# Performance work log

Measured on AMD Instinct MI355X. Metric: run time of the kernel, lower is better.

The kernel has to match this reference:

```python
import jax, jax.numpy as jnp
import numpy as np

B, S, D = 2, 4096, 1024

def setup_inputs() -> dict:
    key = jax.random.key(0)
    k1, k2 = jax.random.split(key)
    x = jax.random.normal(k1, (B, S, D), dtype=jnp.float32)
    W = jax.random.normal(k2, (D, 3 * D), dtype=jnp.float32) * (1.0 / np.sqrt(D))
    b = jnp.zeros((3 * D,), dtype=jnp.float32)
    return {"x": x, "W": W, "b": b}

def reference(x, W, b) -> jnp.ndarray:
    D_ = x.shape[-1]
    qkv = x @ W + b                       # [B, S, 3D]
    q, k, v = jnp.split(qkv, 3, axis=2)    # each [B, S, D]
    scale = 1.0 / jnp.sqrt(jnp.asarray(D_, dtype=x.dtype))
    scores = jnp.einsum('bqd,bkd->bqk', q, k) * scale  # [B, S, S]
    weights = jax.nn.softmax(scores, axis=-1)
    return jnp.einsum('bqk,bkd->bqd', weights, v)       # [B, S, D]
```

## Files before the change

kernel.cpp:

```cpp
#include <hip/hip_runtime.h>
#include <hip/hip_bf16.h>

typedef __attribute__((ext_vector_type(4))) float  f32x4;
typedef __attribute__((ext_vector_type(8))) __bf16 bf16x8;
typedef __attribute__((ext_vector_type(8))) unsigned short u16x8;

typedef const __attribute__((address_space(1))) void gas_void;
typedef __attribute__((address_space(3))) void las_void;

__device__ __forceinline__ unsigned short f2bf(float x) {
    unsigned u = __builtin_bit_cast(unsigned, x);
    u += 0x7fffu + ((u >> 16) & 1u);
    return (unsigned short)(u >> 16);
}
__device__ __forceinline__ float bf2f(unsigned short h) {
    unsigned u = ((unsigned)h) << 16;
    return __builtin_bit_cast(float, u);
}
__device__ __forceinline__ void gload_lds16(const void* g, void* l) {
    __builtin_amdgcn_global_load_lds((gas_void*)g, (las_void*)l, 16, 0, 0);
}

#define WAITVM(N) asm volatile("s_waitcnt vmcnt(" #N ")" ::: "memory")

__global__ void k_f32_to_bf16(const float* __restrict__ in,
                              unsigned short* __restrict__ out, int n4) {
    int i = blockIdx.x * blockDim.x + threadIdx.x;
    if (i < n4) {
        float4 v = ((const float4*)in)[i];
        ushort4 o;
        o.x = f2bf(v.x); o.y = f2bf(v.y); o.z = f2bf(v.z); o.w = f2bf(v.w);
        ((ushort4*)out)[i] = o;
    }
}

__global__ void k_transpose_w(const float* __restrict__ W,
                              unsigned short* __restrict__ Wt,
                              int K, int N) {
    __shared__ unsigned short tile[32][33];
    int n0 = blockIdx.x * 32, k0 = blockIdx.y * 32;
    int tx = threadIdx.x, ty = threadIdx.y;
#pragma unroll
    for (int i = 0; i < 4; i++) {
        int kk = ty + i * 8;
        tile[kk][tx] = f2bf(W[(size_t)(k0 + kk) * N + n0 + tx]);
    }
    __syncthreads();
#pragma unroll
    for (int i = 0; i < 4; i++) {
        int nn = ty + i * 8;
        Wt[(size_t)(n0 + nn) * K + k0 + tx] = tile[tx][nn];
    }
}

__global__ void k_transpose_v(const unsigned short* __restrict__ Vrow,
                              unsigned short* __restrict__ Vt) {
    __shared__ unsigned short tile[32][33];
    int b = blockIdx.z;
    int s0 = blockIdx.x * 32, d0 = blockIdx.y * 32;
    int tx = threadIdx.x, ty = threadIdx.y;
#pragma unroll
    for (int i = 0; i < 4; i++) {
        int ss = ty + i * 8;
        tile[ss][tx] = Vrow[((size_t)(b * 4096 + s0 + ss)) * 1024 + d0 + tx];
    }
    __syncthreads();
#pragma unroll
    for (int i = 0; i < 4; i++) {
        int dd = ty + i * 8;
        Vt[((size_t)b * 1024 + d0 + dd) * 4096 + s0 + tx] = tile[tx][dd];
    }
}

template <int MODE>
__global__ __launch_bounds__(512, 2) void k_g256(
        const unsigned short* __restrict__ A, int lda,
        const unsigned short* __restrict__ Bt, int ldb,
        void* __restrict__ C, int ldc,
        unsigned short* __restrict__ Vp,
        const float* __restrict__ bias,
        int K, float alpha, long sA, long sB, long sC) {
    __shared__ __align__(16) unsigned short As[2][16384];
    __shared__ __align__(16) unsigned short Bs[2][16384];

    const int z = blockIdx.z;
    A  += (size_t)z * sA;
    Bt += (size_t)z * sB;

    const int nwg  = gridDim.x * gridDim.y;
    const int flat = blockIdx.y * gridDim.x + blockIdx.x;
    const int swzb = (flat & 7) * (nwg >> 3) + (flat >> 3);
    const int m0   = (swzb / gridDim.x) * 256;
    const int n0   = (swzb % gridDim.x) * 256;

    const int tid  = threadIdx.x;
    const int lane = tid & 63;
    const int wid  = tid >> 6;
    const int wm   = wid >> 2;
    const int wn   = wid & 3;
    const int l15  = lane & 15;
    const int l4   = lane >> 4;

    f32x4 acc[8][4] = {};

    const int srow = wid * 8 + (lane >> 3);
    const int kel  = (((lane & 7) ^ (lane >> 3)) << 3);
    const int c0 = ((l4 << 4)) ^ ((l15 & 7) << 4);
    const int c1 = (64 + (l4 << 4)) ^ ((l15 & 7) << 4);

    auto stageA = [&](int b, int h, int kt) {
#pragma unroll
        for (int c = 0; c < 2; c++) {
            const int r = h * 128 + c * 64 + srow;
            gload_lds16(A + (size_t)(m0 + r) * lda + kt * 64 + kel,
                        (char*)As + b * 32768 + h * 16384 + c * 8192 + (wid << 10));
        }
    };
    auto stageB = [&](int b, int h, int kt) {
#pragma unroll
        for (int c = 0; c < 2; c++) {
            const int r = h * 128 + c * 64 + srow;
            gload_lds16(Bt + (size_t)(n0 + r) * ldb + kt * 64 + kel,
                        (char*)Bs + b * 32768 + h * 16384 + c * 8192 + (wid << 10));
        }
    };

#define MM(I, J, X, Y) \
    acc[I][J] = __builtin_amdgcn_mfma_f32_16x16x32_bf16((X), (Y), acc[I][J], 0, 0, 0)

    const int NT = K >> 6;
    stageA(0, 0, 0); stageB(0, 0, 0); stageA(0, 1, 0); stageB(0, 1, 0);

    for (int t = 0; t < NT; t++) {
        const int cur = t & 1, nxt = cur ^ 1;
        const char* Ab = (const char*)As + cur * 32768;
        const char* Bb = (const char*)Bs + cur * 32768;

        if (t + 1 < NT) {
            stageA(nxt, 0, t + 1); stageB(nxt, 0, t + 1);
            WAITVM(4);
        } else {
            WAITVM(0);
        }
        __builtin_amdgcn_s_barrier();
        __builtin_amdgcn_sched_barrier(0);

        bf16x8 bfrg[2][2][2];
#pragma unroll
        for (int qn = 0; qn < 2; qn++)
#pragma unroll
        for (int nf = 0; nf < 2; nf++) {
            const int rb = (wn * 64 + qn * 32 + nf * 16 + l15) * 128;
            bfrg[qn][nf][0] = *(const bf16x8*)(Bb + rb + c0);
            bfrg[qn][nf][1] = *(const bf16x8*)(Bb + rb + c1);
        }
        {
            bf16x8 af[4][2];
#pragma unroll
            for (int mf = 0; mf < 4; mf++) {
                const int ra = (wm * 128 + 0 * 64 + mf * 16 + l15) * 128;
                af[mf][0] = *(const bf16x8*)(Ab + ra + c0);
                af[mf][1] = *(const bf16x8*)(Ab + ra + c1);
            }
            __builtin_amdgcn_s_setprio(1);
#pragma unroll
            for (int mf = 0; mf < 4; mf++)
#pragma unroll
            for (int qn = 0; qn < 2; qn++)
#pragma unroll
            for (int nf = 0; nf < 2; nf++) {
                MM(mf, qn * 2 + nf, af[mf][0], bfrg[qn][nf][0]);
                MM(mf, qn * 2 + nf, af[mf][1], bfrg[qn][nf][1]);
            }
            __builtin_amdgcn_s_setprio(0);
        }

        if (t + 1 < NT) { stageA(nxt, 1, t + 1); stageB(nxt, 1, t + 1); }
        {
            bf16x8 af[4][2];
#pragma unroll
            for (int mf = 0; mf < 4; mf++) {
                const int ra = (wm * 128 + 1 * 64 + mf * 16 + l15) * 128;
                af[mf][0] = *(const bf16x8*)(Ab + ra + c0);
                af[mf][1] = *(const bf16x8*)(Ab + ra + c1);
            }
            __builtin_amdgcn_s_setprio(1);
#pragma unroll
            for (int mf = 0; mf < 4; mf++)
#pragma unroll
            for (int qn = 0; qn < 2; qn++)
#pragma unroll
            for (int nf = 0; nf < 2; nf++) {
                MM(4 + mf, qn * 2 + nf, af[mf][0], bfrg[qn][nf][0]);
                MM(4 + mf, qn * 2 + nf, af[mf][1], bfrg[qn][nf][1]);
            }
            __builtin_amdgcn_s_setprio(0);
        }
        __builtin_amdgcn_s_barrier();
        __builtin_amdgcn_sched_barrier(0);
    }
#undef MM

#pragma unroll
    for (int qm = 0; qm < 2; qm++)
#pragma unroll
    for (int mf = 0; mf < 4; mf++) {
        const int row = m0 + wm * 128 + qm * 64 + mf * 16 + l4 * 4;
#pragma unroll
        for (int qn = 0; qn < 2; qn++)
#pragma unroll
        for (int nf = 0; nf < 2; nf++) {
            const int col = n0 + wn * 64 + qn * 32 + nf * 16 + l15;
            const float bv = (MODE == 2) ? bias[col] : 0.0f;
            const f32x4 av = acc[qm * 4 + mf][qn * 2 + nf];
#pragma unroll
            for (int r = 0; r < 4; r++) {
                const float v = av[r] * alpha + bv;
                if (MODE == 1) {
                    ((unsigned short*)C)[(size_t)z * sC + (size_t)(row + r) * ldc + col] = f2bf(v);
                } else {
                    const int lc = col & 1023;
                    if (col < 2048)
                        ((unsigned short*)C)[(size_t)(col >> 10) * 8388608 +
                                             (size_t)(row + r) * 1024 + lc] = f2bf(v);
                    else
                        Vp[(size_t)(row + r) * 1024 + lc] = f2bf(v);
                }
            }
        }
    }
}

__global__ void k_gemm_bt_f32(const unsigned short* __restrict__ A, int lda,
                              const unsigned short* __restrict__ Bt, int ldb,
                              float* __restrict__ C, int ldc,
                              int K, long sA, long sB, long sC) {
    __shared__ __align__(16) unsigned short As[128 * 32];
    __shared__ __align__(16) unsigned short Bs[128 * 32];

    const int z = blockIdx.z;
    A  += (size_t)z * sA;
    Bt += (size_t)z * sB;

    const int nwg  = gridDim.x * gridDim.y;
    const int flat = blockIdx.y * gridDim.x + blockIdx.x;
    const int swzb = (flat & 7) * (nwg >> 3) + (flat >> 3);
    const int m0   = (swzb / gridDim.x) * 128;
    const int n0   = (swzb % gridDim.x) * 128;

    const int tid  = threadIdx.x;
    const int lane = tid & 63;
    const int w    = tid >> 6;
    const int wr   = w >> 1, wc = w & 1;

    f32x4 acc[4][4] = {};
    const int r0  = lane >> 2;
    const int cEl = (lane & 3) * 8;

    for (int k0 = 0; k0 < K; k0 += 32) {
#pragma unroll
        for (int i = 0; i < 2; i++) {
            const int c = w + 4 * i;
            gload_lds16(A + (size_t)(m0 + c * 16 + r0) * lda + k0 + cEl,
                        (void*)(As + c * 512));
        }
#pragma unroll
        for (int i = 0; i < 2; i++) {
            const int c = w + 4 * i;
            gload_lds16(Bt + (size_t)(n0 + c * 16 + r0) * ldb + k0 + cEl,
                        (void*)(Bs + c * 512));
        }
        __syncthreads();

        bf16x8 af[4], bfr[4];
#pragma unroll
        for (int m = 0; m < 4; m++)
            af[m] = *(const bf16x8*)&As[(wr * 64 + m * 16 + (lane & 15)) * 32 + (lane >> 4) * 8];
#pragma unroll
        for (int n = 0; n < 4; n++)
            bfr[n] = *(const bf16x8*)&Bs[(wc * 64 + n * 16 + (lane & 15)) * 32 + (lane >> 4) * 8];

#pragma unroll
        for (int m = 0; m < 4; m++)
#pragma unroll
            for (int n = 0; n < 4; n++)
                acc[m][n] = __builtin_amdgcn_mfma_f32_16x16x32_bf16(af[m], bfr[n], acc[m][n], 0, 0, 0);

        __syncthreads();
    }

#pragma unroll
    for (int m = 0; m < 4; m++) {
        const int row = m0 + wr * 64 + m * 16 + (lane >> 4) * 4;
#pragma unroll
        for (int n = 0; n < 4; n++) {
            const int col = n0 + wc * 64 + n * 16 + (lane & 15);
#pragma unroll
            for (int r = 0; r < 4; r++)
                C[(size_t)z * sC + (size_t)(row + r) * ldc + col] = acc[m][n][r];
        }
    }
}

__global__ __launch_bounds__(256) void k_softmax_inplace(unsigned short* __restrict__ P, int S) {
    __shared__ float red[8];
    const int row  = blockIdx.x;
    const int tid  = threadIdx.x;
    const int lane = tid & 63;
    const int wid  = tid >> 6;
    unsigned short* p = P + (size_t)row * S;

    float v[16];
    u16x8 h0 = *(const u16x8*)&p[tid * 16];
    u16x8 h1 = *(const u16x8*)&p[tid * 16 + 8];
    float mx = -1e30f;
#pragma unroll
    for (int j = 0; j < 8; j++) { v[j]     = bf2f(h0[j]); mx = fmaxf(mx, v[j]);     }
#pragma unroll
    for (int j = 0; j < 8; j++) { v[j + 8] = bf2f(h1[j]); mx = fmaxf(mx, v[j + 8]); }

#pragma unroll
    for (int o = 32; o >= 1; o >>= 1) mx = fmaxf(mx, __shfl_xor(mx, o));
    if (lane == 0) red[wid] = mx;
    __syncthreads();
    mx = fmaxf(fmaxf(red[0], red[1]), fmaxf(red[2], red[3]));

    float sum = 0.0f;
#pragma unroll
    for (int j = 0; j < 16; j++) { v[j] = __expf(v[j] - mx); sum += v[j]; }
#pragma unroll
    for (int o = 32; o >= 1; o >>= 1) sum += __shfl_xor(sum, o);
    if (lane == 0) red[4 + wid] = sum;
    __syncthreads();
    sum = red[4] + red[5] + red[6] + red[7];
    const float rinv = 1.0f / sum;

    u16x8 o0, o1;
#pragma unroll
    for (int j = 0; j < 8; j++) { o0[j] = f2bf(v[j] * rinv); o1[j] = f2bf(v[j + 8] * rinv); }
    *(u16x8*)&p[tid * 16]     = o0;
    *(u16x8*)&p[tid * 16 + 8] = o1;
}

extern "C" void kernel_launch(void* const* d_in, const int* in_sizes, int n_in,
                              void* d_out, int out_size, void* d_ws, size_t ws_size,
                              hipStream_t stream) {
    const float* x    = (const float*)d_in[0];
    const float* W    = (const float*)d_in[1];
    const float* bias = (const float*)d_in[2];
    float* out        = (float*)d_out;

    char* ws = (char*)d_ws;
    unsigned short* Qb   = (unsigned short*)(ws);
    unsigned short* Vt   = (unsigned short*)(ws + 33554432);
    unsigned short* xb   = (unsigned short*)(ws + 50331648);
    unsigned short* Wt   = (unsigned short*)(ws + 67108864);
    unsigned short* Vrow = (unsigned short*)(ws + 73400320);
    unsigned short* Pcat = (unsigned short*)(ws + 50331648);

    k_f32_to_bf16<<<8192, 256, 0, stream>>>(x, xb, (8192 * 1024) / 4);
    k_transpose_w<<<dim3(96, 32), dim3(32, 8), 0, stream>>>(W, Wt, 1024, 3072);
    k_g256<2><<<dim3(12, 32, 1), 512, 0, stream>>>(
        xb, 1024, Wt, 1024, (void*)Qb, 1024, Vrow, bias, 1024, 1.0f, 0, 0, 0);
    k_transpose_v<<<dim3(128, 32, 2), dim3(32, 8), 0, stream>>>(Vrow, Vt);

    const float scale = 0.03125f;
    k_g256<1><<<dim3(16, 16, 2), 512, 0, stream>>>(
        Qb, 1024, Qb + 8388608, 1024, (void*)Pcat, 4096, nullptr, nullptr,
        1024, scale, 4194304, 4194304, 16777216);
    k_softmax_inplace<<<8192, 256, 0, stream>>>(Pcat, 4096);
    k_gemm_bt_f32<<<dim3(8, 32, 2), 256, 0, stream>>>(
        Pcat, 4096, Vt, 4096, out, 1024, 4096, 16777216, 4194304, 4194304);
}
```

Before: 278.8 us.

## Replace PV GEMM with double-buffered 256x128 tile kernel using swizzled LDS

The P·V GEMM is rewritten from a single-buffered 128x128 kernel with BK=32 into a 512-thread kernel that computes a 256x128 tile with BK=64. It double-buffers LDS, issues the next tile's global-to-LDS loads in two halves interleaved with MFMA work, and uses an XOR-swizzled LDS layout plus setprio around the MFMA blocks. The aim is to hide memory latency, raise arithmetic intensity and avoid LDS bank conflicts. In exchange it uses more LDS and registers per block and launches fewer workgroups (256 in total). The srow expression in the existing kernel is also rewritten in an equivalent form.

```diff
diff --git a/kernel.cpp b/kernel.cpp
--- a/kernel.cpp
+++ b/kernel.cpp
@@ -103,7 +103,7 @@
 
     f32x4 acc[8][4] = {};
 
-    const int srow = wid * 8 + (lane >> 3);
+    const int srow = tid >> 3;
     const int kel  = (((lane & 7) ^ (lane >> 3)) << 3);
     const int c0 = ((l4 << 4)) ^ ((l15 & 7) << 4);
     const int c1 = (64 + (l4 << 4)) ^ ((l15 & 7) << 4);
@@ -231,12 +231,13 @@
     }
 }
 
-__global__ void k_gemm_bt_f32(const unsigned short* __restrict__ A, int lda,
-                              const unsigned short* __restrict__ Bt, int ldb,
-                              float* __restrict__ C, int ldc,
-                              int K, long sA, long sB, long sC) {
-    __shared__ __align__(16) unsigned short As[128 * 32];
-    __shared__ __align__(16) unsigned short Bs[128 * 32];
+__global__ __launch_bounds__(512, 2) void k_pv256(
+        const unsigned short* __restrict__ A, int lda,
+        const unsigned short* __restrict__ Bt, int ldb,
+        float* __restrict__ C, int ldc,
+        int K, long sA, long sB, long sC) {
+    __shared__ __align__(16) unsigned short As[2][16384];
+    __shared__ __align__(16) unsigned short Bs[2][8192];
 
     const int z = blockIdx.z;
     A  += (size_t)z * sA;
@@ -245,59 +246,120 @@
     const int nwg  = gridDim.x * gridDim.y;
     const int flat = blockIdx.y * gridDim.x + blockIdx.x;
     const int swzb = (flat & 7) * (nwg >> 3) + (flat >> 3);
-    const int m0   = (swzb / gridDim.x) * 128;
+    const int m0   = (swzb / gridDim.x) * 256;
     const int n0   = (swzb % gridDim.x) * 128;
 
     const int tid  = threadIdx.x;
     const int lane = tid & 63;
-    const int w    = tid >> 6;
-    const int wr   = w >> 1, wc = w & 1;
-
-    f32x4 acc[4][4] = {};
-    const int r0  = lane >> 2;
-    const int cEl = (lane & 3) * 8;
-
-    for (int k0 = 0; k0 < K; k0 += 32) {
-#pragma unroll
-        for (int i = 0; i < 2; i++) {
-            const int c = w + 4 * i;
-            gload_lds16(A + (size_t)(m0 + c * 16 + r0) * lda + k0 + cEl,
-                        (void*)(As + c * 512));
-        }
-#pragma unroll
-        for (int i = 0; i < 2; i++) {
-            const int c = w + 4 * i;
-            gload_lds16(Bt + (size_t)(n0 + c * 16 + r0) * ldb + k0 + cEl,
-                        (void*)(Bs + c * 512));
-        }
-        __syncthreads();
-
-        bf16x8 af[4], bfr[4];
-#pragma unroll
-        for (int m = 0; m < 4; m++)
-            af[m] = *(const bf16x8*)&As[(wr * 64 + m * 16 + (lane & 15)) * 32 + (lane >> 4) * 8];
-#pragma unroll
-        for (int n = 0; n < 4; n++)
-            bfr[n] = *(const bf16x8*)&Bs[(wc * 64 + n * 16 + (lane & 15)) * 32 + (lane >> 4) * 8];
-
-#pragma unroll
-        for (int m = 0; m < 4; m++)
-#pragma unroll
-            for (int n = 0; n < 4; n++)
-                acc[m][n] = __builtin_amdgcn_mfma_f32_16x16x32_bf16(af[m], bfr[n], acc[m][n], 0, 0, 0);
-
-        __syncthreads();
-    }
-
-#pragma unroll
-    for (int m = 0; m < 4; m++) {
-        const int row = m0 + wr * 64 + m * 16 + (lane >> 4) * 4;
-#pragma unroll
-        for (int n = 0; n < 4; n++) {
-            const int col = n0 + wc * 64 + n * 16 + (lane & 15);
+    const int wid  = tid >> 6;
+    const int wm   = wid >> 2;
+    const int wn   = wid & 3;
+    const int l15  = lane & 15;
+    const int l4   = lane >> 4;
+
+    f32x4 acc[8][2] = {};
+
+    const int srow = tid >> 3;
+    const int kel  = (((lane & 7) ^ (lane >> 3)) << 3);
+    const int c0 = ((l4 << 4)) ^ ((l15 & 7) << 4);
+    const int c1 = (64 + (l4 << 4)) ^ ((l15 & 7) << 4);
+
+    auto stageA1 = [&](int b, int a, int kt) {
+        const int r = a * 64 + srow;
+        gload_lds16(A + (size_t)(m0 + r) * lda + kt * 64 + kel,
+                    (char*)As + b * 32768 + a * 8192 + (wid << 10));
+    };
+    auto stageB1 = [&](int b, int c, int kt) {
+        const int r = c * 64 + srow;
+        gload_lds16(Bt + (size_t)(n0 + r) * ldb + kt * 64 + kel,
+                    (char*)Bs + b * 16384 + c * 8192 + (wid << 10));
+    };
+
+#define MM(I, J, X, Y) \
+    acc[I][J] = __builtin_amdgcn_mfma_f32_16x16x32_bf16((X), (Y), acc[I][J], 0, 0, 0)
+
+    const int NT = K >> 6;
+    stageA1(0, 0, 0); stageA1(0, 1, 0); stageA1(0, 2, 0); stageA1(0, 3, 0);
+    stageB1(0, 0, 0); stageB1(0, 1, 0);
+
+    for (int t = 0; t < NT; t++) {
+        const int cur = t & 1, nxt = cur ^ 1;
+        const char* Ab = (const char*)As + cur * 32768;
+        const char* Bb = (const char*)Bs + cur * 16384;
+
+        if (t + 1 < NT) {
+            stageA1(nxt, 0, t + 1); stageA1(nxt, 1, t + 1); stageB1(nxt, 0, t + 1);
+            WAITVM(3);
+        } else {
+            WAITVM(0);
+        }
+        __builtin_amdgcn_s_barrier();
+        __builtin_amdgcn_sched_barrier(0);
+
+        bf16x8 bfrg[2][2];
+#pragma unroll
+        for (int nf = 0; nf < 2; nf++) {
+            const int rb = (wn * 32 + nf * 16 + l15) * 128;
+            bfrg[nf][0] = *(const bf16x8*)(Bb + rb + c0);
+            bfrg[nf][1] = *(const bf16x8*)(Bb + rb + c1);
+        }
+        {
+            bf16x8 af[4][2];
+#pragma unroll
+            for (int mf = 0; mf < 4; mf++) {
+                const int ra = (wm * 128 + 0 * 64 + mf * 16 + l15) * 128;
+                af[mf][0] = *(const bf16x8*)(Ab + ra + c0);
+                af[mf][1] = *(const bf16x8*)(Ab + ra + c1);
+            }
+            __builtin_amdgcn_s_setprio(1);
+#pragma unroll
+            for (int mf = 0; mf < 4; mf++)
+#pragma unroll
+            for (int nf = 0; nf < 2; nf++) {
+                MM(mf, nf, af[mf][0], bfrg[nf][0]);
+                MM(mf, nf, af[mf][1], bfrg[nf][1]);
+            }
+            __builtin_amdgcn_s_setprio(0);
+        }
+
+        if (t + 1 < NT) {
+            stageA1(nxt, 2, t + 1); stageA1(nxt, 3, t + 1); stageB1(nxt, 1, t + 1);
+        }
+        {
+            bf16x8 af[4][2];
+#pragma unroll
+            for (int mf = 0; mf < 4; mf++) {
+                const int ra = (wm * 128 + 1 * 64 + mf * 16 + l15) * 128;
+                af[mf][0] = *(const bf16x8*)(Ab + ra + c0);
+                af[mf][1] = *(const bf16x8*)(Ab + ra + c1);
+            }
+            __builtin_amdgcn_s_setprio(1);
+#pragma unroll
+            for (int mf = 0; mf < 4; mf++)
+#pragma unroll
+            for (int nf = 0; nf < 2; nf++) {
+                MM(4 + mf, nf, af[mf][0], bfrg[nf][0]);
+                MM(4 + mf, nf, af[mf][1], bfrg[nf][1]);
+            }
+            __builtin_amdgcn_s_setprio(0);
+        }
+        __builtin_amdgcn_s_barrier();
+        __builtin_amdgcn_sched_barrier(0);
+    }
+#undef MM
+
+#pragma unroll
+    for (int qm = 0; qm < 2; qm++)
+#pragma unroll
+    for (int mf = 0; mf < 4; mf++) {
+        const int row = m0 + wm * 128 + qm * 64 + mf * 16 + l4 * 4;
+#pragma unroll
+        for (int nf = 0; nf < 2; nf++) {
+            const int col = n0 + wn * 32 + nf * 16 + l15;
+            const f32x4 av = acc[qm * 4 + mf][nf];
 #pragma unroll
             for (int r = 0; r < 4; r++)
-                C[(size_t)z * sC + (size_t)(row + r) * ldc + col] = acc[m][n][r];
+                C[(size_t)z * sC + (size_t)(row + r) * ldc + col] = av[r];
         }
     }
 }
@@ -369,6 +431,6 @@
         Qb, 1024, Qb + 8388608, 1024, (void*)Pcat, 4096, nullptr, nullptr,
         1024, scale, 4194304, 4194304, 16777216);
     k_softmax_inplace<<<8192, 256, 0, stream>>>(Pcat, 4096);
-    k_gemm_bt_f32<<<dim3(8, 32, 2), 256, 0, stream>>>(
+    k_pv256<<<dim3(8, 16, 2), 512, 0, stream>>>(
         Pcat, 4096, Vt, 4096, out, 1024, 4096, 16777216, 4194304, 4194304);
 }
```

Measured after the change: 277.6 us. About the same (-0.4%).
